# Performance work log

Measured on AMD Instinct MI355X. Metric: run time of the kernel, lower is better.

The kernel has to match this reference:

```python
import jax, jax.numpy as jnp
import numpy as np

GN_GROUPS = 32
GN_EPS = 1e-5


def _conv3x3(x, w, b):
    # NCHW 3x3 conv, stride 1, pad 1
    y = jax.lax.conv_general_dilated(x, w, (1, 1), [(1, 1), (1, 1)],
                                     dimension_numbers=('NCHW', 'OIHW', 'NCHW'))
    return y + b[None, :, None, None]


def _bilinear(x, py, px):
    # x: [N,C,H,W]; py,px: [N,H,W] fractional sample coords; zeros outside.
    N, C, H, W = x.shape
    y0 = jnp.floor(py)
    x0 = jnp.floor(px)
    wy = py - y0
    wx = px - x0
    xf = x.reshape(N, C, H * W)
    out = jnp.zeros((N, C, H, W), x.dtype)
    corners = ((y0, x0, (1 - wy) * (1 - wx)),
               (y0, x0 + 1, (1 - wy) * wx),
               (y0 + 1, x0, wy * (1 - wx)),
               (y0 + 1, x0 + 1, wy * wx))
    for yy, xx, w in corners:
        valid = ((yy >= 0) & (yy <= H - 1) & (xx >= 0) & (xx <= W - 1)).astype(x.dtype)
        yi = jnp.clip(yy, 0, H - 1).astype(jnp.int32)
        xi = jnp.clip(xx, 0, W - 1).astype(jnp.int32)
        idx = (yi * W + xi).reshape(N, 1, H * W)
        g = jnp.take_along_axis(xf, idx, axis=2).reshape(N, C, H, W)
        out = out + g * (w * valid)[:, None]
    return out


def setup_inputs() -> dict:
    key = jax.random.key(0)
    ks = jax.random.split(key, 8)
    N, C, H, W = 4, 128, 160, 160
    s = 0.05
    return {
        'x': jax.random.normal(ks[0], (N, C, H, W), jnp.float32),
        'w_tm': jax.random.normal(ks[1], (4, C, 3, 3), jnp.float32) * s,
        'b_tm': jax.random.normal(ks[2], (4,), jnp.float32) * s,
        'w_tr': jax.random.normal(ks[3], (2, C, 3, 3), jnp.float32) * s,
        'b_tr': jax.random.normal(ks[4], (2,), jnp.float32) * s,
        'w_dcn': jax.random.normal(ks[5], (C, C, 3, 3), jnp.float32) * s,
        'gn_gamma': jnp.ones((C,), jnp.float32),
        'gn_beta': jnp.zeros((C,), jnp.float32),
    }


def reference(x, w_tm, b_tm, w_tr, b_tr, w_dcn, gn_gamma, gn_beta):
    N, C, H, W = x.shape
    Cout = w_dcn.shape[0]
    # regular 3x3 grid offsets: row0 = ky, row1 = kx, k ordered ky-major
    R = jnp.array([[-1., -1., -1., 0., 0., 0., 1., 1., 1.],
                   [-1., 0., 1., -1., 0., 1., -1., 0., 1.]], x.dtype)
    tm = _conv3x3(x, w_tm, b_tm)   # [N,4,H,W] -> per-pixel 2x2 affine
    tr = _conv3x3(x, w_tr, b_tr)   # [N,2,H,W] -> per-pixel (dy,dx) translation
    tmm = tm.transpose(0, 2, 3, 1).reshape(N, H, W, 2, 2)
    off = jnp.einsum('nhwij,jk->nhwik', tmm, R) - R  # [N,H,W,2,9]
    dy = off[:, :, :, 0, :] + tr[:, 0][..., None]    # [N,H,W,9]
    dx = off[:, :, :, 1, :] + tr[:, 1][..., None]
    hh = jnp.arange(H, dtype=x.dtype)[None, :, None, None]
    ww = jnp.arange(W, dtype=x.dtype)[None, None, :, None]
    kk = jnp.arange(9)
    ky = (kk // 3).astype(x.dtype)
    kx = (kk % 3).astype(x.dtype)
    py = hh - 1.0 + ky + dy  # stride=1, pad=1, dilation=1
    px = ww - 1.0 + kx + dx
    wk = w_dcn.reshape(Cout, C, 9)
    out = jnp.zeros((N, Cout, H, W), x.dtype)
    for k in range(9):  # fixed small loop over kernel points
        s = _bilinear(x, py[..., k], px[..., k])
        out = out + jnp.einsum('nchw,oc->nohw', s, wk[:, :, k])
    # GroupNorm
    og = out.reshape(N, GN_GROUPS, (Cout // GN_GROUPS) * H * W)
    mu = og.mean(axis=2, keepdims=True)
    var = og.var(axis=2, keepdims=True)
    og = (og - mu) * jax.lax.rsqrt(var + GN_EPS)
    out = og.reshape(N, Cout, H, W) * gn_gamma[None, :, None, None] + gn_beta[None, :, None, None]
    return jax.nn.relu(out + x)
```

## Files before the change

kernel.cpp:

```cpp
#include <hip/hip_runtime.h>
#include <hip/hip_fp16.h>
#include <math.h>

#define Hh 160
#define Ww 160
#define Cc 128
#define HW 25600
#define NPIX 102400

typedef __attribute__((ext_vector_type(8))) _Float16 half8;
typedef __attribute__((ext_vector_type(4))) float f32x4;
typedef __attribute__((ext_vector_type(4))) unsigned int u32x4;

union h2u { __half2 h; unsigned int u; };

#define WS_OFFS 0u
#define WS_WA   7372800u
#define WS_GSUM 7667712u
#define WS_GSQ  7668224u
#define WS_XT   7668736u
#define WS_RAW  33883136u

__global__ void wtrans_kernel(const float* __restrict__ w_dcn,
                              unsigned short* __restrict__ wA) {
    int idx = blockIdx.x * 256 + threadIdx.x;
    if (idx >= 9 * 128 * 128) return;
    int k = idx >> 14;
    int o = (idx >> 7) & 127;
    int c = idx & 127;
    wA[idx] = __half_as_ushort(__float2half(w_dcn[(o * 128 + c) * 9 + k]));
}

__global__ void __launch_bounds__(256) xpose_kernel(
    const float* __restrict__ x, unsigned short* __restrict__ xT) {
    __shared__ float L[128 * 65];
    int bid = blockIdx.x;
    int px0g = 12800 * (bid & 7) + 64 * (bid >> 3);
    int n = px0g / HW;
    int px0 = px0g - n * HW;
    int t = threadIdx.x;
    const float* xn = x + (size_t)n * Cc * HW + px0;
#pragma unroll
    for (int i = 0; i < 32; ++i) {
        int idx = i * 256 + t;
        int ch = idx >> 6;
        int pxl = idx & 63;
        L[ch * 65 + pxl] = xn[(size_t)ch * HW + pxl];
    }
    __syncthreads();
    unsigned short* dst = xT + ((size_t)n * HW + px0) * 128;
#pragma unroll
    for (int j = 0; j < 16; ++j) {
        int idx = j * 256 + t;
        int pxl = idx >> 6;
        int cp = idx & 63;
        h2u cv;
        cv.h = __floats2half2_rn(L[(2 * cp) * 65 + pxl],
                                 L[(2 * cp + 1) * 65 + pxl]);
        *(unsigned int*)(dst + (size_t)pxl * 128 + cp * 2) = cv.u;
    }
}

__global__ void __launch_bounds__(256) offs_kernel(
    const float* __restrict__ x, const float* __restrict__ w_tm,
    const float* __restrict__ b_tm, const float* __restrict__ w_tr,
    const float* __restrict__ b_tr, float* __restrict__ offs2) {
    __shared__ float wt[128 * 9 * 8];
    int t = threadIdx.x;
    for (int idx = t; idx < 6912; idx += 256) {
        int j = idx % 6;
        int rest = idx / 6;
        int tap = rest % 9;
        int c = rest / 9;
        float v = (j < 4) ? w_tm[(j * 128 + c) * 9 + tap]
                          : w_tr[((j - 4) * 128 + c) * 9 + tap];
        wt[rest * 8 + j] = v;
    }
    __syncthreads();
    int bid = blockIdx.x;
    int blk = (bid & 7) * 50 + (bid >> 3);
    int p = blk * 256 + t;
    int n = p / HW;
    int hw = p - n * HW;
    int h = hw / Ww;
    int w = hw - h * Ww;
    int addr[9];
    float msk[9];
#pragma unroll
    for (int tap = 0; tap < 9; ++tap) {
        int dy = tap / 3 - 1, dx = tap % 3 - 1;
        int yy = h + dy, xx = w + dx;
        bool v = (yy >= 0) && (yy < Hh) && (xx >= 0) && (xx < Ww);
        addr[tap] = v ? yy * Ww + xx : 0;
        msk[tap] = v ? 1.f : 0.f;
    }
    float a0 = 0, a1 = 0, a2 = 0, a3 = 0, a4 = 0, a5 = 0;
    const float* xn = x + n * Cc * HW;
#pragma unroll 2
    for (int c = 0; c < Cc; ++c) {
        const float* xc = xn + c * HW;
#pragma unroll
        for (int tap = 0; tap < 9; ++tap) {
            float v = msk[tap] * xc[addr[tap]];
            const float* wp = &wt[(c * 9 + tap) * 8];
            float4 w4 = *(const float4*)wp;
            float2 w2 = *(const float2*)(wp + 4);
            a0 += v * w4.x; a1 += v * w4.y; a2 += v * w4.z; a3 += v * w4.w;
            a4 += v * w2.x; a5 += v * w2.y;
        }
    }
    a0 += b_tm[0]; a1 += b_tm[1]; a2 += b_tm[2]; a3 += b_tm[3];
    a4 += b_tr[0]; a5 += b_tr[1];
#pragma unroll
    for (int k = 0; k < 9; ++k) {
        float r0 = (float)(k / 3) - 1.f;
        float r1 = (float)(k % 3) - 1.f;
        float2 st;
        st.x = (float)h + a0 * r0 + a1 * r1 + a4;
        st.y = (float)w + a2 * r0 + a3 * r1 + a5;
        *(float2*)(offs2 + ((size_t)k * NPIX + p) * 2) = st;
    }
}

__global__ void __launch_bounds__(256, 2) dcn2_kernel(
    const unsigned short* __restrict__ xT, const float* __restrict__ offs2,
    const unsigned short* __restrict__ wA, float* __restrict__ raw,
    float* __restrict__ gsum, float* __restrict__ gsq) {
    __shared__ __align__(16) unsigned short Bt[128 * 128];
    int t = threadIdx.x;
    int lane = t & 63;
    int wid = t >> 6;
    int wm = wid & 1, wn = wid >> 1;
    int quad = lane >> 4, l15 = lane & 15;
    int sub = lane >> 4;
    int s = lane & 15;

    int bid = blockIdx.x;
    int blk = (bid & 7) * 100 + (bid >> 3);
    int px0 = blk * 128;
    int n = px0 / HW;
    int hw0 = px0 - n * HW;
    const unsigned short* xb = xT + (size_t)n * HW * 128;
    const char* Ag = (const char*)wA;
    const float2* offv = (const float2*)offs2;
    int pbase = px0 + wid * 32 + sub;
    int sb = s << 3;

    f32x4 acc[4][4];
#pragma unroll
    for (int i = 0; i < 4; ++i)
#pragma unroll
        for (int j = 0; j < 4; ++j) acc[i][j] = (f32x4)0.f;

    float2 pc[8];
#pragma unroll
    for (int r = 0; r < 8; ++r)
        pc[r] = offv[pbase + r * 4];

    for (int k = 0; k < 9; ++k) {
        __syncthreads();
        float2 pcn[8];
        if (k < 8) {
#pragma unroll
            for (int r = 0; r < 8; ++r)
                pcn[r] = offv[(size_t)(k + 1) * NPIX + pbase + r * 4];
        }
#pragma unroll
        for (int r = 0; r < 8; ++r) {
            int p = wid * 32 + r * 4 + sub;
            float py = pc[r].x, pxx = pc[r].y;
            float y0f = floorf(py), x0f = floorf(pxx);
            float fy = py - y0f, fx = pxx - x0f;
            int y0 = (int)y0f, xi0 = (int)x0f;
            int y1 = y0 + 1, xi1 = xi0 + 1;
            float w00 = (1.f - fy) * (1.f - fx), w01 = (1.f - fy) * fx;
            float w10 = fy * (1.f - fx), w11 = fy * fx;
            bool vy0 = (unsigned)y0 < (unsigned)Hh;
            bool vy1 = (unsigned)y1 < (unsigned)Hh;
            bool vx0 = (unsigned)xi0 < (unsigned)Ww;
            bool vx1 = (unsigned)xi1 < (unsigned)Ww;
            w00 = (vy0 && vx0) ? w00 : 0.f;
            w01 = (vy0 && vx1) ? w01 : 0.f;
            w10 = (vy1 && vx0) ? w10 : 0.f;
            w11 = (vy1 && vx1) ? w11 : 0.f;
            int cy0 = vy0 ? y0 : 0, cy1 = vy1 ? y1 : 0;
            int cx0 = vx0 ? xi0 : 0, cx1 = vx1 ? xi1 : 0;
            u32x4 v00 = *(const u32x4*)(xb + ((size_t)(cy0 * Ww + cx0) << 7) + sb);
            u32x4 v01 = *(const u32x4*)(xb + ((size_t)(cy0 * Ww + cx1) << 7) + sb);
            u32x4 v10 = *(const u32x4*)(xb + ((size_t)(cy1 * Ww + cx0) << 7) + sb);
            u32x4 v11 = *(const u32x4*)(xb + ((size_t)(cy1 * Ww + cx1) << 7) + sb);
            __half2 W00 = __float2half2_rn(w00);
            __half2 W01 = __float2half2_rn(w01);
            __half2 W10 = __float2half2_rn(w10);
            __half2 W11 = __float2half2_rn(w11);
            u32x4 outv;
#pragma unroll
            for (int e = 0; e < 4; ++e) {
                h2u a, b, c, d, o;
                a.u = v00[e]; b.u = v01[e]; c.u = v10[e]; d.u = v11[e];
                __half2 acc2 = __hmul2(W11, d.h);
                acc2 = __hfma2(W10, c.h, acc2);
                acc2 = __hfma2(W01, b.h, acc2);
                acc2 = __hfma2(W00, a.h, acc2);
                o.h = acc2;
                outv[e] = o.u;
            }
            *(u32x4*)&Bt[p * 128 + ((s ^ (p & 15)) << 3)] = outv;
        }
        __syncthreads();

#pragma unroll
        for (int q = 0; q < 4; ++q) {
            half8 a[4], b[4];
#pragma unroll
            for (int i = 0; i < 4; ++i)
                a[i] = *(const half8*)(Ag +
                        ((size_t)(k * 128 + wm * 64 + i * 16 + l15) << 8) +
                        q * 64 + quad * 16);
#pragma unroll
            for (int j = 0; j < 4; ++j) {
                int row = wn * 64 + j * 16 + l15;
                int ur = (q * 4 + quad) ^ (row & 15);
                b[j] = *(const half8*)&Bt[row * 128 + ur * 8];
            }
#pragma unroll
            for (int i = 0; i < 4; ++i)
#pragma unroll
                for (int j = 0; j < 4; ++j)
                    acc[i][j] = __builtin_amdgcn_mfma_f32_16x16x32_f16(
                        a[i], b[j], acc[i][j], 0, 0, 0);
        }

        if (k < 8) {
#pragma unroll
            for (int r = 0; r < 8; ++r) pc[r] = pcn[r];
        }
    }

    size_t rbase = ((size_t)n * Cc) * HW + hw0;
#pragma unroll
    for (int i = 0; i < 4; ++i) {
        float s_i = 0.f, q_i = 0.f;
#pragma unroll
        for (int j = 0; j < 4; ++j) {
            int pxl = wn * 64 + j * 16 + l15;
#pragma unroll
            for (int rr = 0; rr < 4; ++rr) {
                int o = wm * 64 + i * 16 + quad * 4 + rr;
                float v = acc[i][j][rr];
                __builtin_nontemporal_store(v,
                    &raw[rbase + (size_t)o * HW + pxl]);
                s_i += v;
                q_i += v * v;
            }
        }
#pragma unroll
        for (int m = 1; m < 16; m <<= 1) {
            s_i += __shfl_xor(s_i, m);
            q_i += __shfl_xor(q_i, m);
        }
        if (l15 == 0) {
            int g = wm * 16 + i * 4 + quad;
            atomicAdd(&gsum[n * 32 + g], s_i);
            atomicAdd(&gsq[n * 32 + g], q_i);
        }
    }
}

__global__ void __launch_bounds__(256) finish_kernel(
    const float* __restrict__ raw, const float* __restrict__ x,
    const float* __restrict__ gsum, const float* __restrict__ gsq,
    const float* __restrict__ gamma, const float* __restrict__ beta,
    float* __restrict__ out) {
    int i = blockIdx.x * 256 + threadIdx.x;
    int e = i * 4;
    int n = e / (Cc * HW);
    int rem = e - n * (Cc * HW);
    int c = rem / HW;
    int g = c >> 2;
    const float inv = 1.f / 102400.f;
    float mu = gsum[n * 32 + g] * inv;
    float var = gsq[n * 32 + g] * inv - mu * mu;
    float rs = rsqrtf(var + 1e-5f);
    float sc = gamma[c] * rs;
    float sh = beta[c] - mu * sc;
    float4 v = *(const float4*)&raw[e];
    float4 xv = *(const float4*)&x[e];
    float4 r;
    r.x = fmaxf(v.x * sc + sh + xv.x, 0.f);
    r.y = fmaxf(v.y * sc + sh + xv.y, 0.f);
    r.z = fmaxf(v.z * sc + sh + xv.z, 0.f);
    r.w = fmaxf(v.w * sc + sh + xv.w, 0.f);
    *(float4*)&out[e] = r;
}

extern "C" void kernel_launch(void* const* d_in, const int* in_sizes, int n_in,
                              void* d_out, int out_size, void* d_ws, size_t ws_size,
                              hipStream_t stream) {
    const float* x      = (const float*)d_in[0];
    const float* w_tm   = (const float*)d_in[1];
    const float* b_tm   = (const float*)d_in[2];
    const float* w_tr   = (const float*)d_in[3];
    const float* b_tr   = (const float*)d_in[4];
    const float* w_dcn  = (const float*)d_in[5];
    const float* gamma  = (const float*)d_in[6];
    const float* beta   = (const float*)d_in[7];
    char* ws = (char*)d_ws;
    float*          offs2 = (float*)(ws + WS_OFFS);
    unsigned short* wA    = (unsigned short*)(ws + WS_WA);
    float*          gsum  = (float*)(ws + WS_GSUM);
    float*          gsq   = (float*)(ws + WS_GSQ);
    unsigned short* xT    = (unsigned short*)(ws + WS_XT);
    float*          raw   = (float*)(ws + WS_RAW);
    float* out = (float*)d_out;

    (void)hipMemsetAsync(gsum, 0, 1024, stream);
    wtrans_kernel<<<576, 256, 0, stream>>>(w_dcn, wA);
    offs_kernel<<<400, 256, 0, stream>>>(x, w_tm, b_tm, w_tr, b_tr, offs2);
    xpose_kernel<<<1600, 256, 0, stream>>>(x, xT);
    dcn2_kernel<<<800, 256, 0, stream>>>(xT, offs2, wA, raw, gsum, gsq);
    finish_kernel<<<12800, 256, 0, stream>>>(raw, x, gsum, gsq, gamma, beta, out);
}
```

Baseline: 341.7 us.

## Store raw conv output as fp16 and batch bilinear gathers before blending

The raw pre-GroupNorm conv output is now stored as fp16 instead of fp32, which halves the write traffic from the DCN kernel and the read traffic in the finish kernel. The GroupNorm statistics are still summed from the fp32 accumulators. In the DCN kernel, all 32 corner gathers for the 8 pixels are issued before any blending so more global loads are in flight at once. All A-operand fragments for the step are also loaded up front. In exchange, register pressure rises under the 2-waves launch bound, and rounding raw to fp16 adds precision error.

After: 335.1 us. Within noise of the previous version (-1.9%).

```diff
diff --git a/kernel.cpp b/kernel.cpp
--- a/kernel.cpp
+++ b/kernel.cpp
@@ -124,7 +124,7 @@
 
 __global__ void __launch_bounds__(256, 2) dcn2_kernel(
     const unsigned short* __restrict__ xT, const float* __restrict__ offs2,
-    const unsigned short* __restrict__ wA, float* __restrict__ raw,
+    const unsigned short* __restrict__ wA, unsigned short* __restrict__ raw,
     float* __restrict__ gsum, float* __restrict__ gsq) {
     __shared__ __align__(16) unsigned short Bt[128 * 128];
     int t = threadIdx.x;
@@ -152,52 +152,61 @@
 #pragma unroll
         for (int j = 0; j < 4; ++j) acc[i][j] = (f32x4)0.f;
 
-    float2 pc[8];
+    float2 pc[8], pcn[8];
+    u32x4 v00[8], v01[8], v10[8], v11[8];
+    float w00[8], w01[8], w10[8], w11[8];
+
 #pragma unroll
     for (int r = 0; r < 8; ++r)
         pc[r] = offv[pbase + r * 4];
 
     for (int k = 0; k < 9; ++k) {
         __syncthreads();
-        float2 pcn[8];
+
         if (k < 8) {
 #pragma unroll
             for (int r = 0; r < 8; ++r)
                 pcn[r] = offv[(size_t)(k + 1) * NPIX + pbase + r * 4];
         }
+
 #pragma unroll
         for (int r = 0; r < 8; ++r) {
-            int p = wid * 32 + r * 4 + sub;
             float py = pc[r].x, pxx = pc[r].y;
             float y0f = floorf(py), x0f = floorf(pxx);
             float fy = py - y0f, fx = pxx - x0f;
             int y0 = (int)y0f, xi0 = (int)x0f;
             int y1 = y0 + 1, xi1 = xi0 + 1;
-            float w00 = (1.f - fy) * (1.f - fx), w01 = (1.f - fy) * fx;
-            float w10 = fy * (1.f - fx), w11 = fy * fx;
+            float wa = (1.f - fy) * (1.f - fx), wb = (1.f - fy) * fx;
+            float wc = fy * (1.f - fx), wd = fy * fx;
             bool vy0 = (unsigned)y0 < (unsigned)Hh;
             bool vy1 = (unsigned)y1 < (unsigned)Hh;
             bool vx0 = (unsigned)xi0 < (unsigned)Ww;
             bool vx1 = (unsigned)xi1 < (unsigned)Ww;
-            w00 = (vy0 && vx0) ? w00 : 0.f;
-            w01 = (vy0 && vx1) ? w01 : 0.f;
-            w10 = (vy1 && vx0) ? w10 : 0.f;
-            w11 = (vy1 && vx1) ? w11 : 0.f;
+            w00[r] = (vy0 && vx0) ? wa : 0.f;
+            w01[r] = (vy0 && vx1) ? wb : 0.f;
+            w10[r] = (vy1 && vx0) ? wc : 0.f;
+            w11[r] = (vy1 && vx1) ? wd : 0.f;
             int cy0 = vy0 ? y0 : 0, cy1 = vy1 ? y1 : 0;
             int cx0 = vx0 ? xi0 : 0, cx1 = vx1 ? xi1 : 0;
-            u32x4 v00 = *(const u32x4*)(xb + ((size_t)(cy0 * Ww + cx0) << 7) + sb);
-            u32x4 v01 = *(const u32x4*)(xb + ((size_t)(cy0 * Ww + cx1) << 7) + sb);
-            u32x4 v10 = *(const u32x4*)(xb + ((size_t)(cy1 * Ww + cx0) << 7) + sb);
-            u32x4 v11 = *(const u32x4*)(xb + ((size_t)(cy1 * Ww + cx1) << 7) + sb);
-            __half2 W00 = __float2half2_rn(w00);
-            __half2 W01 = __float2half2_rn(w01);
-            __half2 W10 = __float2half2_rn(w10);
-            __half2 W11 = __float2half2_rn(w11);
+            v00[r] = *(const u32x4*)(xb + ((size_t)(cy0 * Ww + cx0) << 7) + sb);
+            v01[r] = *(const u32x4*)(xb + ((size_t)(cy0 * Ww + cx1) << 7) + sb);
+            v10[r] = *(const u32x4*)(xb + ((size_t)(cy1 * Ww + cx0) << 7) + sb);
+            v11[r] = *(const u32x4*)(xb + ((size_t)(cy1 * Ww + cx1) << 7) + sb);
+        }
+
+#pragma unroll
+        for (int r = 0; r < 8; ++r) {
+            int p = wid * 32 + r * 4 + sub;
+            __half2 W00 = __float2half2_rn(w00[r]);
+            __half2 W01 = __float2half2_rn(w01[r]);
+            __half2 W10 = __float2half2_rn(w10[r]);
+            __half2 W11 = __float2half2_rn(w11[r]);
             u32x4 outv;
 #pragma unroll
             for (int e = 0; e < 4; ++e) {
                 h2u a, b, c, d, o;
-                a.u = v00[e]; b.u = v01[e]; c.u = v10[e]; d.u = v11[e];
+                a.u = v00[r][e]; b.u = v01[r][e];
+                c.u = v10[r][e]; d.u = v11[r][e];
                 __half2 acc2 = __hmul2(W11, d.h);
                 acc2 = __hfma2(W10, c.h, acc2);
                 acc2 = __hfma2(W01, b.h, acc2);
@@ -209,14 +218,17 @@
         }
         __syncthreads();
 
-#pragma unroll
-        for (int q = 0; q < 4; ++q) {
-            half8 a[4], b[4];
+        half8 a[4][4];
+#pragma unroll
+        for (int q = 0; q < 4; ++q)
 #pragma unroll
             for (int i = 0; i < 4; ++i)
-                a[i] = *(const half8*)(Ag +
+                a[q][i] = *(const half8*)(Ag +
                         ((size_t)(k * 128 + wm * 64 + i * 16 + l15) << 8) +
                         q * 64 + quad * 16);
+#pragma unroll
+        for (int q = 0; q < 4; ++q) {
+            half8 b[4];
 #pragma unroll
             for (int j = 0; j < 4; ++j) {
                 int row = wn * 64 + j * 16 + l15;
@@ -228,7 +240,7 @@
 #pragma unroll
                 for (int j = 0; j < 4; ++j)
                     acc[i][j] = __builtin_amdgcn_mfma_f32_16x16x32_f16(
-                        a[i], b[j], acc[i][j], 0, 0, 0);
+                        a[q][i], b[j], acc[i][j], 0, 0, 0);
         }
 
         if (k < 8) {
@@ -248,8 +260,8 @@
             for (int rr = 0; rr < 4; ++rr) {
                 int o = wm * 64 + i * 16 + quad * 4 + rr;
                 float v = acc[i][j][rr];
-                __builtin_nontemporal_store(v,
-                    &raw[rbase + (size_t)o * HW + pxl]);
+                raw[rbase + (size_t)o * HW + pxl] =
+                    __half_as_ushort(__float2half(v));
                 s_i += v;
                 q_i += v * v;
             }
@@ -268,7 +280,7 @@
 }
 
 __global__ void __launch_bounds__(256) finish_kernel(
-    const float* __restrict__ raw, const float* __restrict__ x,
+    const unsigned short* __restrict__ raw, const float* __restrict__ x,
     const float* __restrict__ gsum, const float* __restrict__ gsq,
     const float* __restrict__ gamma, const float* __restrict__ beta,
     float* __restrict__ out) {
@@ -284,13 +296,15 @@
     float rs = rsqrtf(var + 1e-5f);
     float sc = gamma[c] * rs;
     float sh = beta[c] - mu * sc;
-    float4 v = *(const float4*)&raw[e];
+    const __half2* rh = (const __half2*)raw;
+    __half2 p01 = rh[i * 2];
+    __half2 p23 = rh[i * 2 + 1];
     float4 xv = *(const float4*)&x[e];
     float4 r;
-    r.x = fmaxf(v.x * sc + sh + xv.x, 0.f);
-    r.y = fmaxf(v.y * sc + sh + xv.y, 0.f);
-    r.z = fmaxf(v.z * sc + sh + xv.z, 0.f);
-    r.w = fmaxf(v.w * sc + sh + xv.w, 0.f);
+    r.x = fmaxf(__low2float(p01)  * sc + sh + xv.x, 0.f);
+    r.y = fmaxf(__high2float(p01) * sc + sh + xv.y, 0.f);
+    r.z = fmaxf(__low2float(p23)  * sc + sh + xv.z, 0.f);
+    r.w = fmaxf(__high2float(p23) * sc + sh + xv.w, 0.f);
     *(float4*)&out[e] = r;
 }
 
@@ -311,7 +325,7 @@
     float*          gsum  = (float*)(ws + WS_GSUM);
     float*          gsq   = (float*)(ws + WS_GSQ);
     unsigned short* xT    = (unsigned short*)(ws + WS_XT);
-    float*          raw   = (float*)(ws + WS_RAW);
+    unsigned short* raw   = (unsigned short*)(ws + WS_RAW);
     float* out = (float*)d_out;
 
     (void)hipMemsetAsync(gsum, 0, 1024, stream);
```
